# Kernel tuning notes

Hardware: AMD Instinct MI355X
Metric: run time of the kernel (lower is better)

The kernel has to match this reference:

```python
import jax, jax.numpy as jnp
import numpy as np

N_FEAT = 7          # input_vector_size
M = 3               # memberships per feature (hardcoded 3 in torch module)
FUZZ = M ** N_FEAT  # 2187, cartesian product size
MID = 512
NUM_CLASS = 10
BATCH = 4096

# Precompute cartesian-product index table: itertools.product over rows of u[i]
# (last feature index varies fastest). IDX[k, i] = which of the 3 memberships of
# feature i appears in combination k.
_k = np.arange(FUZZ)
IDX = ((_k[:, None] // (M ** np.arange(N_FEAT - 1, -1, -1))[None, :]) % M).astype(np.int32)  # [FUZZ, N_FEAT]


def setup_inputs() -> dict:
    key = jax.random.key(0)
    ks = jax.random.split(key, 8)
    x = jax.random.normal(ks[0], (BATCH, N_FEAT), dtype=jnp.float32)
    # Parameters (xavier-ish init for weights, ones for b/bais as in torch init)
    c = jax.random.uniform(ks[1], (N_FEAT, M), minval=-1.0, maxval=1.0, dtype=jnp.float32)
    b = jnp.ones((N_FEAT, M), dtype=jnp.float32)
    wei = jax.random.uniform(ks[2], (FUZZ * N_FEAT, FUZZ), minval=-0.01, maxval=0.01, dtype=jnp.float32)
    bais = jnp.ones((1,), dtype=jnp.float32)
    W1 = jax.random.normal(ks[3], (MID, FUZZ), dtype=jnp.float32) * (1.0 / np.sqrt(FUZZ))
    b1 = jnp.zeros((MID,), dtype=jnp.float32)
    W2 = jax.random.normal(ks[4], (FUZZ, MID), dtype=jnp.float32) * (1.0 / np.sqrt(MID))
    b2 = jnp.zeros((FUZZ,), dtype=jnp.float32)
    W3 = jax.random.normal(ks[5], (NUM_CLASS, FUZZ), dtype=jnp.float32) * (1.0 / np.sqrt(FUZZ))
    b3 = jnp.zeros((NUM_CLASS,), dtype=jnp.float32)
    return {"x": x, "c": c, "b": b, "wei": wei, "bais": bais,
            "W1": W1, "b1": b1, "W2": W2, "b2": b2, "W3": W3, "b3": b3}


def reference(x, c, b, wei, bais, W1, b1, W2, b2, W3, b3):
    B = x.shape[0]
    # Gaussian fuzzy memberships: u[b, i, j] = exp(-(x[b,i]-c[i,j])^2 / b[i,j]^2)
    u = jnp.exp(-((x[:, :, None] - c[None]) ** 2) / (b[None] ** 2))  # [B, N_FEAT, M]
    # Cartesian product: dd[bt, k, i] = u[bt, i, IDX[k, i]]  (replaces itertools.product)
    idx = jnp.asarray(IDX)                       # [FUZZ, N_FEAT]
    feat = jnp.arange(N_FEAT)[None, :]           # [1, N_FEAT] broadcasts to [FUZZ, N_FEAT]
    dd = u[:, feat, idx]                         # [B, FUZZ, N_FEAT]
    # Fuzzy rule layer
    a = dd.reshape(B, FUZZ * N_FEAT) @ wei + bais            # [B, FUZZ]
    a_mean = a / jnp.sum(a, axis=1, keepdims=True)
    # Small residual MLP
    h1 = a_mean @ W1.T + b1                                   # [B, MID]
    h2 = h1 @ W2.T + b2                                       # [B, FUZZ]
    h3 = (a_mean + h2) @ W3.T + b3                            # [B, NUM_CLASS]
    out = jax.nn.leaky_relu(h3, negative_slope=0.2)
    # Dropout(0.5) omitted (eval mode / deterministic baseline)
    return out
```

## Files before the change

### kernel.cpp

```cpp
#include <hip/hip_runtime.h>

#define FUZZ 2187
#define NFEAT 7
#define MID 512
#define NCLS 10
#define BATCH 4096
#define SSTR 2192

constexpr int pw3(int e) { int r = 1; while (e--) r *= 3; return r; }

template<int J>
__device__ __forceinline__ float group_range(const float* __restrict__ wei,
                                             int m, int n, int e0, int cnt) {
    constexpr int PL = pw3(6 - J);
    float acc = 0.f;
    int e = e0;
    int eend = e0 + cnt;
    while (e + 13 <= eend) {
        float v[13];
#pragma unroll
        for (int u = 0; u < 13; ++u) {
            int ee = e + u;
            int hi = ee / PL;
            int lo = ee - hi * PL;
            int k  = (hi * 3 + m) * PL + lo;
            v[u] = wei[((size_t)k * 7 + J) * FUZZ + n];
        }
#pragma unroll
        for (int u = 0; u < 13; ++u) acc += v[u];
        e += 13;
    }
    while (e < eend) {
        int hi = e / PL;
        int lo = e - hi * PL;
        int k  = (hi * 3 + m) * PL + lo;
        acc += wei[((size_t)k * 7 + J) * FUZZ + n];
        ++e;
    }
    return acc;
}

__global__ __launch_bounds__(512) void k_reduce_wei(const float* __restrict__ wei,
                                                    float* __restrict__ S,
                                                    float* __restrict__ Kz) {
    int g = blockIdx.y;
    int tid = threadIdx.x;
    int w = tid >> 6, lane = tid & 63;
    if (g == 0 && blockIdx.x == 0) {
        for (int z = tid; z < NCLS * MID + 288; z += 512) Kz[z] = 0.f;
    }
    int n = blockIdx.x * 64 + lane;
    int j = g / 3, m = g % 3;
    float acc = 0.f;
    int e0 = w * 91;
    int cnt = (w == 7) ? 92 : 91;
    if (n < FUZZ) {
        switch (j) {
            case 0: acc = group_range<0>(wei, m, n, e0, cnt); break;
            case 1: acc = group_range<1>(wei, m, n, e0, cnt); break;
            case 2: acc = group_range<2>(wei, m, n, e0, cnt); break;
            case 3: acc = group_range<3>(wei, m, n, e0, cnt); break;
            case 4: acc = group_range<4>(wei, m, n, e0, cnt); break;
            case 5: acc = group_range<5>(wei, m, n, e0, cnt); break;
            default: acc = group_range<6>(wei, m, n, e0, cnt); break;
        }
    }
    __shared__ float red[8][64];
    red[w][lane] = acc;
    __syncthreads();
    if (w == 0 && n < FUZZ) {
        float s = 0.f;
#pragma unroll
        for (int ww = 0; ww < 8; ++ww) s += red[ww][lane];
        S[g * SSTR + n] = s;
    }
}

__device__ __forceinline__ float wave_sum(float v) {
#pragma unroll
    for (int off = 32; off > 0; off >>= 1) v += __shfl_down(v, off, 64);
    return v;
}

__global__ __launch_bounds__(256) void k_sw1(const float* __restrict__ S,
                                             const float* __restrict__ W1,
                                             const float* __restrict__ W2,
                                             const float* __restrict__ W3,
                                             float* __restrict__ SW1,
                                             float* __restrict__ ws1,
                                             float* __restrict__ K) {
    int gid = blockIdx.x;
    int tid = threadIdx.x;
    if (gid >= MID) {
        int idx = gid - MID;
        int c = idx / 27;
        int chunk = idx % 27;
        int n0 = chunk * 81;
        float acc0 = 0.f, acc1 = 0.f;
        const float* w3row = W3 + (size_t)c * FUZZ;
        const float* w2col = W2 + tid;
#pragma unroll 9
        for (int n = n0; n < n0 + 81; ++n) {
            float w3 = w3row[n];
            acc0 += w3 * w2col[(size_t)n * MID];
            acc1 += w3 * w2col[(size_t)n * MID + 256];
        }
        atomicAdd(&K[c * MID + tid],       acc0);
        atomicAdd(&K[c * MID + tid + 256], acc1);
        return;
    }
    int i = gid;
    float acc[21];
    float aw = 0.f;
#pragma unroll
    for (int t = 0; t < 21; ++t) acc[t] = 0.f;
    const float* w1row = W1 + (size_t)i * FUZZ;
    for (int n = tid; n < FUZZ; n += 256) {
        float w1 = w1row[n];
        aw += w1;
#pragma unroll
        for (int t = 0; t < 21; ++t) acc[t] += S[t * SSTR + n] * w1;
    }
#pragma unroll
    for (int t = 0; t < 21; ++t) acc[t] = wave_sum(acc[t]);
    aw = wave_sum(aw);
    __shared__ float red[4][22];
    int w = tid >> 6, lane = tid & 63;
    if (lane == 0) {
#pragma unroll
        for (int t = 0; t < 21; ++t) red[w][t] = acc[t];
        red[w][21] = aw;
    }
    __syncthreads();
    if (tid < 22) {
        float s = red[0][tid] + red[1][tid] + red[2][tid] + red[3][tid];
        if (tid < 21) SW1[tid * MID + i] = s;
        else          ws1[i] = s;
    }
}

__global__ __launch_bounds__(64) void k_h(const float* __restrict__ S,
                                          const float* __restrict__ SW1,
                                          const float* __restrict__ ws1,
                                          const float* __restrict__ K,
                                          const float* __restrict__ b1,
                                          const float* __restrict__ b2,
                                          const float* __restrict__ b3,
                                          const float* __restrict__ W3,
                                          float* __restrict__ H,
                                          float* __restrict__ v,
                                          float* __restrict__ w,
                                          float* __restrict__ T) {
    int c = blockIdx.x;
    int chunk = blockIdx.y;
    int lane = threadIdx.x;
    int n0 = chunk * 243;
    if (c < NCLS) {
        float acc[21];
        float av = 0.f, aw = 0.f;
#pragma unroll
        for (int t = 0; t < 21; ++t) acc[t] = 0.f;
        const float* w3row = W3 + (size_t)c * FUZZ;
        for (int n = n0 + lane; n < n0 + 243; n += 64) {
            float w3 = w3row[n];
            av += w3;
            aw += b2[n] * w3;
#pragma unroll
            for (int t = 0; t < 21; ++t)
                acc[t] += S[t * SSTR + n] * w3;
        }
        if (chunk < 8) {
            int i = chunk * 64 + lane;
            float kk = K[c * MID + i];
            av += ws1[i] * kk;
            aw += b1[i] * kk;
#pragma unroll
            for (int t = 0; t < 21; ++t)
                acc[t] += SW1[t * MID + i] * kk;
        }
#pragma unroll
        for (int t = 0; t < 21; ++t) acc[t] = wave_sum(acc[t]);
        av = wave_sum(av);
        aw = wave_sum(aw);
        if (lane == 0) {
#pragma unroll
            for (int t = 0; t < 21; ++t) atomicAdd(&H[t * NCLS + c], acc[t]);
            atomicAdd(&v[c], av);
            atomicAdd(&w[c], aw + (chunk == 0 ? b3[c] : 0.f));
        }
    } else {
        float acc[21];
#pragma unroll
        for (int t = 0; t < 21; ++t) acc[t] = 0.f;
        for (int n = n0 + lane; n < n0 + 243; n += 64) {
#pragma unroll
            for (int t = 0; t < 21; ++t) acc[t] += S[t * SSTR + n];
        }
#pragma unroll
        for (int t = 0; t < 21; ++t) acc[t] = wave_sum(acc[t]);
        if (lane == 0) {
#pragma unroll
            for (int t = 0; t < 21; ++t) atomicAdd(&T[t], acc[t]);
        }
    }
}

__global__ __launch_bounds__(64) void k_out(const float* __restrict__ x,
                                            const float* __restrict__ cc,
                                            const float* __restrict__ bbv,
                                            const float* __restrict__ bais,
                                            const float* __restrict__ T,
                                            const float* __restrict__ H,
                                            const float* __restrict__ v,
                                            const float* __restrict__ w,
                                            float* __restrict__ out) {
    int b = blockIdx.x * 64 + threadIdx.x;
    if (b >= BATCH) return;
    float xv[NFEAT];
#pragma unroll
    for (int j = 0; j < NFEAT; ++j) xv[j] = x[b * NFEAT + j];
    float u[21];
#pragma unroll
    for (int j = 0; j < NFEAT; ++j) {
#pragma unroll
        for (int m = 0; m < 3; ++m) {
            float d = xv[j] - cc[j * 3 + m];
            float bv = bbv[j * 3 + m];
            u[j * 3 + m] = expf(-(d * d) / (bv * bv));
        }
    }
    float ba = bais[0];
    float r = 2187.0f * ba;
#pragma unroll
    for (int t = 0; t < 21; ++t) r += u[t] * T[t];
    float inv = 1.0f / r;
#pragma unroll
    for (int c = 0; c < NCLS; ++c) {
        float s = 0.f;
#pragma unroll
        for (int t = 0; t < 21; ++t) s += u[t] * H[t * NCLS + c];
        float h = (s + ba * v[c]) * inv + w[c];
        out[b * NCLS + c] = (h >= 0.f) ? h : 0.2f * h;
    }
}

extern "C" void kernel_launch(void* const* d_in, const int* in_sizes, int n_in,
                              void* d_out, int out_size, void* d_ws, size_t ws_size,
                              hipStream_t stream) {
    const float* x    = (const float*)d_in[0];
    const float* c    = (const float*)d_in[1];
    const float* bbv  = (const float*)d_in[2];
    const float* wei  = (const float*)d_in[3];
    const float* bais = (const float*)d_in[4];
    const float* W1   = (const float*)d_in[5];
    const float* b1   = (const float*)d_in[6];
    const float* W2   = (const float*)d_in[7];
    const float* b2   = (const float*)d_in[8];
    const float* W3   = (const float*)d_in[9];
    const float* b3   = (const float*)d_in[10];

    float* ws  = (float*)d_ws;
    float* S   = ws;
    float* K   = S + 21 * SSTR;
    float* T   = K + NCLS * MID;
    float* H   = T + 32;
    float* v   = H + 224;
    float* w   = v + 16;
    float* SW1 = w + 16;
    float* ws1 = SW1 + 21 * MID;

    k_reduce_wei<<<dim3(35, 21), 512, 0, stream>>>(wei, S, K);
    k_sw1<<<MID + 270, 256, 0, stream>>>(S, W1, W2, W3, SW1, ws1, K);
    k_h<<<dim3(NCLS + 1, 9), 64, 0, stream>>>(S, SW1, ws1, K, b1, b2, b3, W3,
                                              H, v, w, T);
    k_out<<<(BATCH + 63) / 64, 64, 0, stream>>>(x, c, bbv, bais, T, H, v, w,
                                                (float*)d_out);
}
```

Baseline: 251.6 us.

## Fold W1/W2/W3 chain into effective W3 and fuse K into reduce kernel

Computes K = W3·W2 inside the wei-reduction launch (extra blockIdx.y rows), then folds K·W1 + W3 into a single effective weight W3E per class. The k_h kernel then contracts S against W3E alone, dropping the 21×512 SW1 product over W1 and its per-row reductions. This reorders the linear algebra so W1 is read once as a 10×512 contraction rather than multiplied against all 21 S rows. It also removes the K atomics and the zeroing of K.

```diff
diff --git a/kernel.cpp b/kernel.cpp
--- a/kernel.cpp
+++ b/kernel.cpp
@@ -41,13 +41,50 @@
 }
 
 __global__ __launch_bounds__(512) void k_reduce_wei(const float* __restrict__ wei,
+                                                    const float* __restrict__ W2,
+                                                    const float* __restrict__ W3,
                                                     float* __restrict__ S,
-                                                    float* __restrict__ Kz) {
-    int g = blockIdx.y;
+                                                    float* __restrict__ K,
+                                                    float* __restrict__ THvw) {
     int tid = threadIdx.x;
     int w = tid >> 6, lane = tid & 63;
+    __shared__ float red[8][64];
+
+    if (blockIdx.y < 3) {
+        int kb = blockIdx.y * 35 + blockIdx.x;
+        if (kb >= 80) return;
+        int c = kb >> 3;
+        int i = (kb & 7) * 64 + lane;
+        int start = w * 273 + (w < 3 ? w : 3);
+        int cnt = 273 + (w < 3 ? 1 : 0);
+        const float* w3row = W3 + (size_t)c * FUZZ;
+        const float* w2col = W2 + i;
+        float acc = 0.f;
+        int n = start, nend = start + cnt;
+        while (n + 13 <= nend) {
+            float vv[13];
+#pragma unroll
+            for (int u = 0; u < 13; ++u)
+                vv[u] = w2col[(size_t)(n + u) * MID];
+#pragma unroll
+            for (int u = 0; u < 13; ++u) acc += vv[u] * w3row[n + u];
+            n += 13;
+        }
+        while (n < nend) { acc += w2col[(size_t)n * MID] * w3row[n]; ++n; }
+        red[w][lane] = acc;
+        __syncthreads();
+        if (w == 0) {
+            float s = 0.f;
+#pragma unroll
+            for (int ww = 0; ww < 8; ++ww) s += red[ww][lane];
+            K[(size_t)c * MID + i] = s;
+        }
+        return;
+    }
+
+    int g = blockIdx.y - 3;
     if (g == 0 && blockIdx.x == 0) {
-        for (int z = tid; z < NCLS * MID + 288; z += 512) Kz[z] = 0.f;
+        if (tid < 288) THvw[tid] = 0.f;
     }
     int n = blockIdx.x * 64 + lane;
     int j = g / 3, m = g % 3;
@@ -65,7 +102,6 @@
             default: acc = group_range<6>(wei, m, n, e0, cnt); break;
         }
     }
-    __shared__ float red[8][64];
     red[w][lane] = acc;
     __syncthreads();
     if (w == 0 && n < FUZZ) {
@@ -82,116 +118,79 @@
     return v;
 }
 
-__global__ __launch_bounds__(256) void k_sw1(const float* __restrict__ S,
-                                             const float* __restrict__ W1,
-                                             const float* __restrict__ W2,
-                                             const float* __restrict__ W3,
-                                             float* __restrict__ SW1,
-                                             float* __restrict__ ws1,
-                                             float* __restrict__ K) {
-    int gid = blockIdx.x;
+__global__ __launch_bounds__(512) void k_w3eff(const float* __restrict__ K,
+                                               const float* __restrict__ W1,
+                                               const float* __restrict__ W3,
+                                               const float* __restrict__ b1,
+                                               const float* __restrict__ b2,
+                                               const float* __restrict__ b3,
+                                               float* __restrict__ W3E,
+                                               float* __restrict__ v,
+                                               float* __restrict__ w) {
+    int c = blockIdx.y;
+    int bx = blockIdx.x;
     int tid = threadIdx.x;
-    if (gid >= MID) {
-        int idx = gid - MID;
-        int c = idx / 27;
-        int chunk = idx % 27;
-        int n0 = chunk * 81;
-        float acc0 = 0.f, acc1 = 0.f;
-        const float* w3row = W3 + (size_t)c * FUZZ;
-        const float* w2col = W2 + tid;
-#pragma unroll 9
-        for (int n = n0; n < n0 + 81; ++n) {
-            float w3 = w3row[n];
-            acc0 += w3 * w2col[(size_t)n * MID];
-            acc1 += w3 * w2col[(size_t)n * MID + 256];
-        }
-        atomicAdd(&K[c * MID + tid],       acc0);
-        atomicAdd(&K[c * MID + tid + 256], acc1);
-        return;
-    }
-    int i = gid;
-    float acc[21];
-    float aw = 0.f;
-#pragma unroll
-    for (int t = 0; t < 21; ++t) acc[t] = 0.f;
-    const float* w1row = W1 + (size_t)i * FUZZ;
-    for (int n = tid; n < FUZZ; n += 256) {
-        float w1 = w1row[n];
-        aw += w1;
-#pragma unroll
-        for (int t = 0; t < 21; ++t) acc[t] += S[t * SSTR + n] * w1;
-    }
-#pragma unroll
-    for (int t = 0; t < 21; ++t) acc[t] = wave_sum(acc[t]);
-    aw = wave_sum(aw);
-    __shared__ float red[4][22];
-    int w = tid >> 6, lane = tid & 63;
-    if (lane == 0) {
-#pragma unroll
-        for (int t = 0; t < 21; ++t) red[w][t] = acc[t];
-        red[w][21] = aw;
-    }
+    int wv = tid >> 6, lane = tid & 63;
+    int n = bx * 64 + lane;
+    bool nok = (n < FUZZ);
+    const float* krow = K + (size_t)c * MID;
+    float acc = 0.f;
+    if (nok) {
+        int i0 = wv * 64;
+        const float* w1p = W1 + (size_t)i0 * FUZZ + n;
+#pragma unroll 8
+        for (int u = 0; u < 64; ++u)
+            acc += krow[i0 + u] * w1p[(size_t)u * FUZZ];
+    }
+    __shared__ float red[8][64];
+    red[wv][lane] = acc;
     __syncthreads();
-    if (tid < 22) {
-        float s = red[0][tid] + red[1][tid] + red[2][tid] + red[3][tid];
-        if (tid < 21) SW1[tid * MID + i] = s;
-        else          ws1[i] = s;
+    if (wv == 0) {
+        float s = 0.f;
+#pragma unroll
+        for (int ww = 0; ww < 8; ++ww) s += red[ww][lane];
+        float w3e = nok ? (s + W3[(size_t)c * FUZZ + n]) : 0.f;
+        if (nok) W3E[(size_t)c * FUZZ + n] = w3e;
+        float vs = wave_sum(w3e);
+        if (lane == 0) atomicAdd(&v[c], vs);
+    } else if (wv == 1) {
+        float ws = nok ? b2[n] * W3[(size_t)c * FUZZ + n] : 0.f;
+        ws = wave_sum(ws);
+        if (lane == 0) atomicAdd(&w[c], ws);
+    } else if (wv == 2 && bx == 0) {
+        float bs = 0.f;
+        for (int i = lane; i < MID; i += 64) bs += b1[i] * krow[i];
+        bs = wave_sum(bs);
+        if (lane == 0) atomicAdd(&w[c], bs + b3[c]);
     }
 }
 
 __global__ __launch_bounds__(64) void k_h(const float* __restrict__ S,
-                                          const float* __restrict__ SW1,
-                                          const float* __restrict__ ws1,
-                                          const float* __restrict__ K,
-                                          const float* __restrict__ b1,
-                                          const float* __restrict__ b2,
-                                          const float* __restrict__ b3,
-                                          const float* __restrict__ W3,
+                                          const float* __restrict__ W3E,
                                           float* __restrict__ H,
-                                          float* __restrict__ v,
-                                          float* __restrict__ w,
                                           float* __restrict__ T) {
     int c = blockIdx.x;
     int chunk = blockIdx.y;
     int lane = threadIdx.x;
     int n0 = chunk * 243;
+    float acc[21];
+#pragma unroll
+    for (int t = 0; t < 21; ++t) acc[t] = 0.f;
     if (c < NCLS) {
-        float acc[21];
-        float av = 0.f, aw = 0.f;
-#pragma unroll
-        for (int t = 0; t < 21; ++t) acc[t] = 0.f;
-        const float* w3row = W3 + (size_t)c * FUZZ;
+        const float* w3row = W3E + (size_t)c * FUZZ;
         for (int n = n0 + lane; n < n0 + 243; n += 64) {
             float w3 = w3row[n];
-            av += w3;
-            aw += b2[n] * w3;
 #pragma unroll
             for (int t = 0; t < 21; ++t)
                 acc[t] += S[t * SSTR + n] * w3;
         }
-        if (chunk < 8) {
-            int i = chunk * 64 + lane;
-            float kk = K[c * MID + i];
-            av += ws1[i] * kk;
-            aw += b1[i] * kk;
-#pragma unroll
-            for (int t = 0; t < 21; ++t)
-                acc[t] += SW1[t * MID + i] * kk;
-        }
 #pragma unroll
         for (int t = 0; t < 21; ++t) acc[t] = wave_sum(acc[t]);
-        av = wave_sum(av);
-        aw = wave_sum(aw);
         if (lane == 0) {
 #pragma unroll
             for (int t = 0; t < 21; ++t) atomicAdd(&H[t * NCLS + c], acc[t]);
-            atomicAdd(&v[c], av);
-            atomicAdd(&w[c], aw + (chunk == 0 ? b3[c] : 0.f));
         }
     } else {
-        float acc[21];
-#pragma unroll
-        for (int t = 0; t < 21; ++t) acc[t] = 0.f;
         for (int n = n0 + lane; n < n0 + 243; n += 64) {
 #pragma unroll
             for (int t = 0; t < 21; ++t) acc[t] += S[t * SSTR + n];
@@ -261,18 +260,17 @@
 
     float* ws  = (float*)d_ws;
     float* S   = ws;
-    float* K   = S + 21 * SSTR;
-    float* T   = K + NCLS * MID;
+    float* T   = S + 21 * SSTR;
     float* H   = T + 32;
     float* v   = H + 224;
     float* w   = v + 16;
-    float* SW1 = w + 16;
-    float* ws1 = SW1 + 21 * MID;
-
-    k_reduce_wei<<<dim3(35, 21), 512, 0, stream>>>(wei, S, K);
-    k_sw1<<<MID + 270, 256, 0, stream>>>(S, W1, W2, W3, SW1, ws1, K);
-    k_h<<<dim3(NCLS + 1, 9), 64, 0, stream>>>(S, SW1, ws1, K, b1, b2, b3, W3,
-                                              H, v, w, T);
+    float* K   = w + 16;
+    float* W3E = K + NCLS * MID;
+
+    k_reduce_wei<<<dim3(35, 24), 512, 0, stream>>>(wei, W2, W3, S, K, T);
+    k_w3eff<<<dim3(35, NCLS), 512, 0, stream>>>(K, W1, W3, b1, b2, b3,
+                                                W3E, v, w);
+    k_h<<<dim3(NCLS + 1, 9), 64, 0, stream>>>(S, W3E, H, T);
     k_out<<<(BATCH + 63) / 64, 64, 0, stream>>>(x, c, bbv, bais, T, H, v, w,
                                                 (float*)d_out);
 }
```

After: 255.3 us. Within noise of the previous version (+1.5%).
